# Kernel tuning notes

Measured on AMD Instinct MI355X. Metric: run time of the kernel, lower is better.

Reference implementation:

```python
import jax, jax.numpy as jnp
import numpy as np

N_SAMPLES = 4_194_304  # total packed samples across all rays
NUM_CLASSES = 32
NUM_RAYS = 131_072


def setup_inputs() -> dict:
    key = jax.random.key(0)
    k1, k2, k3 = jax.random.split(key, 3)
    semantics = jax.random.normal(k1, (N_SAMPLES, NUM_CLASSES), dtype=jnp.float32)
    weights = jax.random.uniform(k2, (N_SAMPLES, 1), dtype=jnp.float32)
    # nerfacc packs samples ray-by-ray, so ray_indices is sorted
    ray_indices = jnp.sort(jax.random.randint(k3, (N_SAMPLES,), 0, NUM_RAYS, dtype=jnp.int64))
    return {
        "semantics": semantics,
        "weights": weights,
        "ray_indices": ray_indices,
        "num_rays": NUM_RAYS,
    }


def reference(semantics, weights, ray_indices, num_rays):
    # nerfacc.accumulate_along_rays: out[r] = sum_{i: ray_indices[i]==r} weights[i,0] * semantics[i]
    vals = weights * semantics  # [N, C], fused multiply
    return jax.ops.segment_sum(vals, ray_indices, num_segments=num_rays)  # [num_rays, C]
```

## Files before the change

### kernel.cpp

```cpp
#include <hip/hip_runtime.h>


typedef float f32x4 __attribute__((ext_vector_type(4)));

__global__ __launch_bounds__(256) void sr_bounds_kernel(
    const int* __restrict__ ridx, int2* __restrict__ seg, int N)
{
    const int t  = blockIdx.x * blockDim.x + threadIdx.x;
    const int i4 = t * 4;
    if (i4 >= N) return;

    if (i4 + 4 <= N) {
        const int4 v = *reinterpret_cast<const int4*>(ridx + i4);
        const int prev = (i4 == 0) ? -1 : ridx[i4 - 1];
        const int tail = (i4 + 4 < N) ? ridx[i4 + 4] : -2;
        if (v.x != prev) { seg[v.x].x = i4;     if (prev >= 0) seg[prev].y = i4; }
        if (v.y != v.x)  { seg[v.y].x = i4 + 1; seg[v.x].y = i4 + 1; }
        if (v.z != v.y)  { seg[v.z].x = i4 + 2; seg[v.y].y = i4 + 2; }
        if (v.w != v.z)  { seg[v.w].x = i4 + 3; seg[v.z].y = i4 + 3; }
        if (v.w != tail) { seg[v.w].y = i4 + 4; }
    } else {
        for (int i = i4; i < N; ++i) {
            const int r    = ridx[i];
            const int prev = (i == 0) ? -1 : ridx[i - 1];
            const int next = (i == N - 1) ? -2 : ridx[i + 1];
            if (r != prev) seg[r].x = i;
            if (r != next) seg[r].y = i + 1;
        }
    }
}

__global__ __launch_bounds__(256) void SemanticRenderer_70205535421052_kernel(
    const f32x4* __restrict__ sem4,
    const float* __restrict__ w,
    const int2*  __restrict__ seg,
    f32x4*       __restrict__ out4,
    int R)
{
    const int wave = threadIdx.x >> 6;
    const int lane = threadIdx.x & 63;
    const int q    = lane & 7;
    const int g    = lane >> 3;
    const int nw   = gridDim.x * 4;
    int r = blockIdx.x * 4 + wave;
    if (r >= R) return;

    int2 se_next = seg[r];

    while (true) {
        const int2 se = se_next;
        const int  rn = r + nw;
        if (rn < R) se_next = seg[rn];
        int s = se.x + g;
        const int e = se.y;
        f32x4 acc = (f32x4)0.f;

        for (; s + 24 < e; s += 32) {
            const float w0 = __builtin_nontemporal_load(w + s);
            const float w1 = __builtin_nontemporal_load(w + s + 8);
            const float w2 = __builtin_nontemporal_load(w + s + 16);
            const float w3 = __builtin_nontemporal_load(w + s + 24);
            const f32x4 v0 = __builtin_nontemporal_load(sem4 + (size_t)s * 8 + q);
            const f32x4 v1 = __builtin_nontemporal_load(sem4 + (size_t)(s + 8)  * 8 + q);
            const f32x4 v2 = __builtin_nontemporal_load(sem4 + (size_t)(s + 16) * 8 + q);
            const f32x4 v3 = __builtin_nontemporal_load(sem4 + (size_t)(s + 24) * 8 + q);
            acc += w0 * v0; acc += w1 * v1; acc += w2 * v2; acc += w3 * v3;
        }
        for (; s + 8 < e; s += 16) {
            const float w0 = __builtin_nontemporal_load(w + s);
            const float w1 = __builtin_nontemporal_load(w + s + 8);
            const f32x4 v0 = __builtin_nontemporal_load(sem4 + (size_t)s * 8 + q);
            const f32x4 v1 = __builtin_nontemporal_load(sem4 + (size_t)(s + 8) * 8 + q);
            acc += w0 * v0; acc += w1 * v1;
        }
        if (s < e) {
            const float w0 = __builtin_nontemporal_load(w + s);
            const f32x4 v0 = __builtin_nontemporal_load(sem4 + (size_t)s * 8 + q);
            acc += w0 * v0;
        }

        #pragma unroll
        for (int m = 8; m < 64; m <<= 1) {
            acc.x += __shfl_xor(acc.x, m, 64);
            acc.y += __shfl_xor(acc.y, m, 64);
            acc.z += __shfl_xor(acc.z, m, 64);
            acc.w += __shfl_xor(acc.w, m, 64);
        }

        if (g == 0)
            __builtin_nontemporal_store(acc, out4 + (size_t)r * 8 + q);

        if (rn >= R) break;
        r = rn;
    }
}

extern "C" void kernel_launch(void* const* d_in, const int* in_sizes, int n_in,
                              void* d_out, int out_size, void* d_ws, size_t ws_size,
                              hipStream_t stream) {
    const f32x4* sem4 = (const f32x4*)d_in[0];
    const float* w    = (const float*)d_in[1];
    const int*   ridx = (const int*)d_in[2];
    f32x4*       out4 = (f32x4*)d_out;

    const int N = in_sizes[1];
    const int R = out_size / 32;

    int2* seg = (int2*)d_ws;

    hipMemsetAsync(seg, 0, (size_t)R * sizeof(int2), stream);

    const int bthreads = (N + 3) / 4;
    sr_bounds_kernel<<<(bthreads + 255) / 256, 256, 0, stream>>>(ridx, seg, N);

    int blocks = 2048;
    const int needed = (R + 3) / 4;
    if (needed < blocks) blocks = needed;
    SemanticRenderer_70205535421052_kernel<<<blocks, 256, 0, stream>>>(
        sem4, w, seg, out4, R);
}
```

Measured before the change: 122.6 us.

## Replace segment-bounds pass with per-wave sample chunks and ballot-based segment detection

Drops the separate bounds kernel and its workspace memset. Each wave now takes a fixed chunk of 256 samples and finds segment boundaries with ballots over the sorted ray indices. Segments that continue across chunk edges are combined with atomicAdd, and interior segments use plain stores. The output must now be zeroed with a memset of the full output, and atomics add some contention and nondeterminism at chunk edges.

```diff
diff --git a/kernel.cpp b/kernel.cpp
--- a/kernel.cpp
+++ b/kernel.cpp
@@ -3,59 +3,75 @@
 
 typedef float f32x4 __attribute__((ext_vector_type(4)));
 
-__global__ __launch_bounds__(256) void sr_bounds_kernel(
-    const int* __restrict__ ridx, int2* __restrict__ seg, int N)
-{
-    const int t  = blockIdx.x * blockDim.x + threadIdx.x;
-    const int i4 = t * 4;
-    if (i4 >= N) return;
-
-    if (i4 + 4 <= N) {
-        const int4 v = *reinterpret_cast<const int4*>(ridx + i4);
-        const int prev = (i4 == 0) ? -1 : ridx[i4 - 1];
-        const int tail = (i4 + 4 < N) ? ridx[i4 + 4] : -2;
-        if (v.x != prev) { seg[v.x].x = i4;     if (prev >= 0) seg[prev].y = i4; }
-        if (v.y != v.x)  { seg[v.y].x = i4 + 1; seg[v.x].y = i4 + 1; }
-        if (v.z != v.y)  { seg[v.z].x = i4 + 2; seg[v.y].y = i4 + 2; }
-        if (v.w != v.z)  { seg[v.w].x = i4 + 3; seg[v.z].y = i4 + 3; }
-        if (v.w != tail) { seg[v.w].y = i4 + 4; }
-    } else {
-        for (int i = i4; i < N; ++i) {
-            const int r    = ridx[i];
-            const int prev = (i == 0) ? -1 : ridx[i - 1];
-            const int next = (i == N - 1) ? -2 : ridx[i + 1];
-            if (r != prev) seg[r].x = i;
-            if (r != next) seg[r].y = i + 1;
-        }
-    }
-}
+#define CHUNK 256
 
 __global__ __launch_bounds__(256) void SemanticRenderer_70205535421052_kernel(
     const f32x4* __restrict__ sem4,
     const float* __restrict__ w,
-    const int2*  __restrict__ seg,
-    f32x4*       __restrict__ out4,
-    int R)
+    const int*   __restrict__ ridx,
+    float*       __restrict__ out,
+    int N)
 {
     const int wave = threadIdx.x >> 6;
     const int lane = threadIdx.x & 63;
     const int q    = lane & 7;
     const int g    = lane >> 3;
-    const int nw   = gridDim.x * 4;
-    int r = blockIdx.x * 4 + wave;
-    if (r >= R) return;
+    const int wid  = blockIdx.x * 4 + wave;
+    const int base = wid * CHUNK;
+    if (base >= N) return;
+    const int CL = min(CHUNK, N - base);
 
-    int2 se_next = seg[r];
+    int4 v;
+    if (CL == CHUNK) {
+        v = *reinterpret_cast<const int4*>(ridx + base + 4 * lane);
+    } else {
+        const int i0 = min(4 * lane,     CL - 1);
+        const int i1 = min(4 * lane + 1, CL - 1);
+        const int i2 = min(4 * lane + 2, CL - 1);
+        const int i3 = min(4 * lane + 3, CL - 1);
+        v.x = ridx[base + i0]; v.y = ridx[base + i1];
+        v.z = ridx[base + i2]; v.w = ridx[base + i3];
+    }
+    const int prev_id = (base > 0)      ? ridx[base - 1]  : -1;
+    const int next_id = (base + CL < N) ? ridx[base + CL] : -1;
 
-    while (true) {
-        const int2 se = se_next;
-        const int  rn = r + nw;
-        if (rn < R) se_next = seg[rn];
-        int s = se.x + g;
-        const int e = se.y;
+    const int leftw = __shfl_up(v.w, 1, 64);
+    const int lft   = (lane == 0) ? prev_id : leftw;
+    const unsigned long long m0 = __ballot(v.x != lft);
+    const unsigned long long m1 = __ballot(v.y != v.x);
+    const unsigned long long m2 = __ballot(v.z != v.y);
+    const unsigned long long m3 = __ballot(v.w != v.z);
+
+    int a = 0;
+    while (a < CL) {
+        int t = CL;
+        {
+            const int h = (a + 4) >> 2;
+            const unsigned long long mm = (h < 64) ? (m0 >> h) : 0ULL;
+            if (mm) { const int c = 4 * (h + __builtin_ctzll(mm));     if (c < t) t = c; }
+        }
+        {
+            const int h = (a + 3) >> 2;
+            const unsigned long long mm = (h < 64) ? (m1 >> h) : 0ULL;
+            if (mm) { const int c = 4 * (h + __builtin_ctzll(mm)) + 1; if (c < t) t = c; }
+        }
+        {
+            const int h = (a + 2) >> 2;
+            const unsigned long long mm = (h < 64) ? (m2 >> h) : 0ULL;
+            if (mm) { const int c = 4 * (h + __builtin_ctzll(mm)) + 2; if (c < t) t = c; }
+        }
+        {
+            const int h = (a + 1) >> 2;
+            const unsigned long long mm = (h < 64) ? (m3 >> h) : 0ULL;
+            if (mm) { const int c = 4 * (h + __builtin_ctzll(mm)) + 3; if (c < t) t = c; }
+        }
+        const int b   = t;
+        const int rid = ridx[base + a];
+
         f32x4 acc = (f32x4)0.f;
-
-        for (; s + 24 < e; s += 32) {
+        int o = a + g;
+        for (; o + 24 < b; o += 32) {
+            const int s = base + o;
             const float w0 = __builtin_nontemporal_load(w + s);
             const float w1 = __builtin_nontemporal_load(w + s + 8);
             const float w2 = __builtin_nontemporal_load(w + s + 16);
@@ -66,14 +82,16 @@
             const f32x4 v3 = __builtin_nontemporal_load(sem4 + (size_t)(s + 24) * 8 + q);
             acc += w0 * v0; acc += w1 * v1; acc += w2 * v2; acc += w3 * v3;
         }
-        for (; s + 8 < e; s += 16) {
+        for (; o + 8 < b; o += 16) {
+            const int s = base + o;
             const float w0 = __builtin_nontemporal_load(w + s);
             const float w1 = __builtin_nontemporal_load(w + s + 8);
             const f32x4 v0 = __builtin_nontemporal_load(sem4 + (size_t)s * 8 + q);
             const f32x4 v1 = __builtin_nontemporal_load(sem4 + (size_t)(s + 8) * 8 + q);
             acc += w0 * v0; acc += w1 * v1;
         }
-        if (s < e) {
+        if (o < b) {
+            const int s = base + o;
             const float w0 = __builtin_nontemporal_load(w + s);
             const f32x4 v0 = __builtin_nontemporal_load(sem4 + (size_t)s * 8 + q);
             acc += w0 * v0;
@@ -87,11 +105,20 @@
             acc.w += __shfl_xor(acc.w, m, 64);
         }
 
-        if (g == 0)
-            __builtin_nontemporal_store(acc, out4 + (size_t)r * 8 + q);
-
-        if (rn >= R) break;
-        r = rn;
+        const bool headcont = (a == 0)  && (rid == prev_id);
+        const bool tailcont = (b == CL) && (rid == next_id);
+        if (g == 0) {
+            float* dst = out + (size_t)rid * 32 + q * 4;
+            if (headcont | tailcont) {
+                atomicAdd(dst + 0, acc.x);
+                atomicAdd(dst + 1, acc.y);
+                atomicAdd(dst + 2, acc.z);
+                atomicAdd(dst + 3, acc.w);
+            } else {
+                __builtin_nontemporal_store(acc, reinterpret_cast<f32x4*>(dst));
+            }
+        }
+        a = b;
     }
 }
 
@@ -101,21 +128,14 @@
     const f32x4* sem4 = (const f32x4*)d_in[0];
     const float* w    = (const float*)d_in[1];
     const int*   ridx = (const int*)d_in[2];
-    f32x4*       out4 = (f32x4*)d_out;
+    float*       out  = (float*)d_out;
 
     const int N = in_sizes[1];
-    const int R = out_size / 32;
 
-    int2* seg = (int2*)d_ws;
+    hipMemsetAsync(out, 0, (size_t)out_size * sizeof(float), stream);
 
-    hipMemsetAsync(seg, 0, (size_t)R * sizeof(int2), stream);
-
-    const int bthreads = (N + 3) / 4;
-    sr_bounds_kernel<<<(bthreads + 255) / 256, 256, 0, stream>>>(ridx, seg, N);
-
-    int blocks = 2048;
-    const int needed = (R + 3) / 4;
-    if (needed < blocks) blocks = needed;
+    const int chunks = (N + CHUNK - 1) / CHUNK;
+    const int blocks = (chunks + 3) / 4;
     SemanticRenderer_70205535421052_kernel<<<blocks, 256, 0, stream>>>(
-        sem4, w, seg, out4, R);
+        sem4, w, ridx, out, N);
 }
```

Result: no change. 125.0 us (+1.9%).
